# Kernel optimization log

Hardware: AMD Instinct MI355X
Metric: run time of the kernel (lower is better)

The kernel has to match this reference:

```python
import jax, jax.numpy as jnp
import numpy as np

B, T, D, H = 2, 4096, 768, 12
DH = D // H


def setup_inputs() -> dict:
    key = jax.random.key(0)
    ks = jax.random.split(key, 4)
    x = jax.random.normal(ks[0], (B, T, D), dtype=jnp.float32)
    Wqkv = jax.random.normal(ks[1], (D, 3 * D), dtype=jnp.float32) * (D ** -0.5)
    bqkv = jnp.zeros((3 * D,), dtype=jnp.float32)
    Wproj = jax.random.normal(ks[2], (D, D), dtype=jnp.float32) * (D ** -0.5)
    bproj = jnp.zeros((D,), dtype=jnp.float32)
    return {"x": x, "Wqkv": Wqkv, "bqkv": bqkv, "Wproj": Wproj, "bproj": bproj}


def reference(x, Wqkv, bqkv, Wproj, bproj):
    b, t, c = x.shape
    qkv = x @ Wqkv + bqkv                      # [B,T,3D]
    qkv = qkv.reshape(b, t, H, 3 * DH)
    q, k, v = jnp.split(qkv, 3, axis=-1)       # each [B,T,H,DH]
    q = q.transpose(0, 2, 1, 3)                # [B,H,T,DH]
    k = k.transpose(0, 2, 1, 3)
    v = v.transpose(0, 2, 1, 3)
    att = jnp.einsum('bhqd,bhkd->bhqk', q, k) / (DH ** 0.5)  # [B,H,T,T]
    mask = jnp.tril(jnp.ones((t, t), dtype=bool))
    att = jnp.where(mask, att, jnp.float32(-1e9))
    att = jax.nn.softmax(att, axis=-1)
    out = jnp.einsum('bhqk,bhkd->bhqd', att, v)  # [B,H,T,DH]
    out = out.transpose(0, 2, 1, 3).reshape(b, t, c)
    return out @ Wproj + bproj
```

## Files before the change

### kernel.cpp

```cpp
#include <hip/hip_runtime.h>

typedef unsigned short u16;
typedef unsigned int u32;
typedef __bf16 bf16x8 __attribute__((ext_vector_type(8)));
typedef float f32x4 __attribute__((ext_vector_type(4)));
typedef float f32x16 __attribute__((ext_vector_type(16)));
typedef u16 u16x4 __attribute__((ext_vector_type(4)));
typedef u32 u32x2 __attribute__((ext_vector_type(2)));
typedef u32 u32x4 __attribute__((ext_vector_type(4)));

#define QSCALE 0.18033688011112042f

static __device__ __forceinline__ u16 f2bf(float f) {
  __bf16 h = (__bf16)f;
  return __builtin_bit_cast(u16, h);
}

static __device__ __forceinline__ u32 pk2(float a, float b) {
  return (u32)f2bf(a) | ((u32)f2bf(b) << 16);
}

static __device__ __forceinline__ void gl_lds16(const void* g, void* l) {
  __builtin_amdgcn_global_load_lds(
      (const __attribute__((address_space(1))) unsigned int*)g,
      (__attribute__((address_space(3))) unsigned int*)l, 16, 0, 0);
}

static __device__ __forceinline__ f32x16 zero16() {
  f32x16 z;
#pragma unroll
  for (int i = 0; i < 16; ++i) z[i] = 0.f;
  return z;
}

__global__ void k_cvt(const float* __restrict__ in, u16* __restrict__ out, int n4) {
  int i = blockIdx.x * 256 + threadIdx.x;
  if (i < n4) {
    f32x4 f = ((const f32x4*)in)[i];
    u16x4 u = { f2bf(f[0]), f2bf(f[1]), f2bf(f[2]), f2bf(f[3]) };
    ((u16x4*)out)[i] = u;
  }
}

__global__ void k_transpose_cvt(const float* __restrict__ in, u16* __restrict__ out,
                                int R, int C) {
  __shared__ float tile[32][33];
  const int c0 = blockIdx.x * 32, r0 = blockIdx.y * 32;
  const int tx = threadIdx.x, ty = threadIdx.y;
#pragma unroll
  for (int i = 0; i < 4; ++i)
    tile[ty + i * 8][tx] = in[(size_t)(r0 + ty + i * 8) * C + c0 + tx];
  __syncthreads();
#pragma unroll
  for (int i = 0; i < 4; ++i)
    out[(size_t)(c0 + ty + i * 8) * R + r0 + tx] = f2bf(tile[tx][ty + i * 8]);
}

static __device__ __forceinline__ void gemm_core(const u16* __restrict__ Ag,
                                                 const u16* __restrict__ Btg,
                                                 int K, int m0, int n0,
                                                 u16* As, u16* Bs,
                                                 f32x4 acc[4][4]) {
  const int tid = threadIdx.x;
  const int lane = tid & 63;
  const int wid = tid >> 6;
  const int wm = wid >> 1, wn = wid & 1;
  const int l16 = lane & 15, lg = lane >> 4;

  for (int kt = 0; kt < K; kt += 64) {
    __syncthreads();
#pragma unroll
    for (int i = 0; i < 4; ++i) {
      int chunk = i * 256 + tid;
      int row = chunk >> 3;
      int lcb = ((chunk & 7) << 4) ^ ((row & 7) << 4);
      gl_lds16(Ag + (size_t)(m0 + row) * K + kt + (lcb >> 1),
               As + ((i * 256 + wid * 64) << 3));
    }
#pragma unroll
    for (int i = 0; i < 4; ++i) {
      int chunk = i * 256 + tid;
      int row = chunk >> 3;
      int lcb = ((chunk & 7) << 4) ^ ((row & 7) << 4);
      gl_lds16(Btg + (size_t)(n0 + row) * K + kt + (lcb >> 1),
               Bs + ((i * 256 + wid * 64) << 3));
    }
    __syncthreads();

#pragma unroll
    for (int ks = 0; ks < 2; ++ks) {
      bf16x8 af[4], bfr[4];
#pragma unroll
      for (int mi = 0; mi < 4; ++mi) {
        int row = wm * 64 + mi * 16 + l16;
        int off = row * 128 + ((ks * 64 + (lg << 4)) ^ ((row & 7) << 4));
        af[mi] = *(const bf16x8*)((const char*)As + off);
      }
#pragma unroll
      for (int ni = 0; ni < 4; ++ni) {
        int row = wn * 64 + ni * 16 + l16;
        int off = row * 128 + ((ks * 64 + (lg << 4)) ^ ((row & 7) << 4));
        bfr[ni] = *(const bf16x8*)((const char*)Bs + off);
      }
#pragma unroll
      for (int mi = 0; mi < 4; ++mi)
#pragma unroll
        for (int ni = 0; ni < 4; ++ni)
          acc[mi][ni] = __builtin_amdgcn_mfma_f32_16x16x32_bf16(
              af[mi], bfr[ni], acc[mi][ni], 0, 0, 0);
    }
  }
}

__global__ __launch_bounds__(256) void k_gemm_qkv(
    const u16* __restrict__ A, const u16* __restrict__ Bt,
    const float* __restrict__ bias, u16* __restrict__ Q, u16* __restrict__ Kb,
    u16* __restrict__ Vt) {
  __shared__ __align__(16) u16 As[128 * 64];
  __shared__ __align__(16) u16 Bs[128 * 64];
  const int m0 = blockIdx.y * 128, n0 = blockIdx.x * 128;
  const f32x4 fz = {0.f, 0.f, 0.f, 0.f};
  f32x4 acc[4][4];
#pragma unroll
  for (int mi = 0; mi < 4; ++mi)
#pragma unroll
    for (int ni = 0; ni < 4; ++ni) acc[mi][ni] = fz;

  gemm_core(A, Bt, 768, m0, n0, As, Bs, acc);

  const int tid = threadIdx.x, lane = tid & 63, wid = tid >> 6;
  const int wm = wid >> 1, wn = wid & 1, l16 = lane & 15, lg = lane >> 4;
#pragma unroll
  for (int mi = 0; mi < 4; ++mi)
#pragma unroll
    for (int ni = 0; ni < 4; ++ni) {
      int n = n0 + wn * 64 + ni * 16 + l16;
      float bi = bias[n];
      int h = n / 192;
      int rr = n - h * 192;
      int m0w = m0 + wm * 64 + mi * 16 + lg * 4;
      int bb = m0w >> 12, t0 = m0w & 4095;
      size_t base = ((size_t)(bb * 12 + h) * 4096 + t0) * 64;
      if (rr < 64) {
#pragma unroll
        for (int r = 0; r < 4; ++r)
          Q[base + (size_t)r * 64 + rr] = f2bf((acc[mi][ni][r] + bi) * QSCALE);
      } else if (rr < 128) {
#pragma unroll
        for (int r = 0; r < 4; ++r)
          Kb[base + (size_t)r * 64 + rr - 64] = f2bf(acc[mi][ni][r] + bi);
      } else {
        u16x4 vv;
#pragma unroll
        for (int r = 0; r < 4; ++r) vv[r] = f2bf(acc[mi][ni][r] + bi);
        *(u16x4*)(Vt + ((size_t)(bb * 12 + h) * 64 + (rr - 128)) * 4096 + t0) = vv;
      }
    }
}

__global__ __launch_bounds__(256) void k_gemm_proj(
    const u16* __restrict__ A, const u16* __restrict__ Bt,
    const float* __restrict__ bias, float* __restrict__ out) {
  __shared__ __align__(16) u16 As[128 * 64];
  __shared__ __align__(16) u16 Bs[128 * 64];
  const int m0 = blockIdx.y * 128, n0 = blockIdx.x * 128;
  const f32x4 fz = {0.f, 0.f, 0.f, 0.f};
  f32x4 acc[4][4];
#pragma unroll
  for (int mi = 0; mi < 4; ++mi)
#pragma unroll
    for (int ni = 0; ni < 4; ++ni) acc[mi][ni] = fz;

  gemm_core(A, Bt, 768, m0, n0, As, Bs, acc);

  const int tid = threadIdx.x, lane = tid & 63, wid = tid >> 6;
  const int wm = wid >> 1, wn = wid & 1, l16 = lane & 15, lg = lane >> 4;
#pragma unroll
  for (int mi = 0; mi < 4; ++mi)
#pragma unroll
    for (int ni = 0; ni < 4; ++ni) {
      int n = n0 + wn * 64 + ni * 16 + l16;
      float bi = bias[n];
#pragma unroll
      for (int r = 0; r < 4; ++r) {
        int m = m0 + wm * 64 + mi * 16 + lg * 4 + r;
        out[(size_t)m * 768 + n] = acc[mi][ni][r] + bi;
      }
    }
}

__global__ __launch_bounds__(128) void k_attn(const u16* __restrict__ Qg,
                                              const u16* __restrict__ Kg,
                                              const u16* __restrict__ Vtg,
                                              u16* __restrict__ Og) {
  __shared__ __align__(16) u16 Ks[2][64 * 64];
  __shared__ __align__(16) u16 Vs[2][64 * 64];
  const int bid = blockIdx.x;
  const int xcd = bid & 7;
  const int g = bid >> 3;
  const int bh = xcd * 3 + (g >> 6);
  const int jX = 63 - (g & 63);
  const int tid = threadIdx.x;
  const int lane = tid & 63;
  const int wid = tid >> 6;
  const int l32 = lane & 31;
  const int hi = lane >> 5;
  const int rxor = (l32 & 7) << 4;
  const size_t qk_base = (size_t)bh * (4096 * 64);
  const size_t vt_base = (size_t)bh * (64 * 4096);
  const int b = bh / 12, h = bh - b * 12;

  const int q0w = jX * 64 + wid * 32;
  const int qrow = q0w + l32;
  const int nkt = jX + 1;

  int coK[4], coVa[4], coVb[4];
#pragma unroll
  for (int st = 0; st < 4; ++st) coK[st] = (st * 32 + hi * 16) ^ rxor;
#pragma unroll
  for (int ks = 0; ks < 4; ++ks) {
    coVa[ks] = (ks * 32 + hi * 8) ^ rxor;
    coVb[ks] = (ks * 32 + 16 + hi * 8) ^ rxor;
  }
  const int rb0 = l32 * 128, rb1 = (32 + l32) * 128;

  const int trow = tid >> 3;
  const int tcol = ((((tid & 7) << 4) ^ ((trow & 7) << 4)) >> 1);
  const int tdst = tid << 3;
  const u16* kp0 = Kg + qk_base + (size_t)trow * 64 + tcol;
  const u16* kp1 = kp0 + (size_t)16 * 64;
  const u16* kp2 = kp0 + (size_t)32 * 64;
  const u16* kp3 = kp0 + (size_t)48 * 64;
  const u16* vq0 = Vtg + vt_base + (size_t)trow * 4096 + tcol;
  const u16* vq1 = vq0 + (size_t)16 * 4096;
  const u16* vq2 = vq0 + (size_t)32 * 4096;
  const u16* vq3 = vq0 + (size_t)48 * 4096;

  auto stage = [&](u16* Kd, u16* Vd) {
    gl_lds16(kp0, Kd + tdst);
    gl_lds16(kp1, Kd + 1024 + tdst);
    gl_lds16(kp2, Kd + 2048 + tdst);
    gl_lds16(kp3, Kd + 3072 + tdst);
    gl_lds16(vq0, Vd + tdst);
    gl_lds16(vq1, Vd + 1024 + tdst);
    gl_lds16(vq2, Vd + 2048 + tdst);
    gl_lds16(vq3, Vd + 3072 + tdst);
    kp0 += 4096; kp1 += 4096; kp2 += 4096; kp3 += 4096;
    vq0 += 64; vq1 += 64; vq2 += 64; vq3 += 64;
  };

  bf16x8 qb[4];
#pragma unroll
  for (int st = 0; st < 4; ++st)
    qb[st] = *(const bf16x8*)(Qg + qk_base + (size_t)qrow * 64 + st * 16 + hi * 8);

  f32x16 o0 = zero16(), o1 = zero16();
  float mrun = -3.0e38f, lrun = 0.f;

  stage(Ks[0], Vs[0]);
  __syncthreads();

  int cur = 0;
  for (int kt = 0; kt < nkt; ++kt) {
    if (kt + 1 < nkt) {
      stage(Ks[cur ^ 1], Vs[cur ^ 1]);
    }
    const bool diag = (kt == nkt - 1);
    const bool halfskip = diag && (wid == 0);
    const char* Kbp = (const char*)Ks[cur];
    const char* Vb = (const char*)Vs[cur];

    f32x16 s0 = zero16(), s1 = zero16();
    __builtin_amdgcn_s_setprio(1);
#pragma unroll
    for (int st = 0; st < 4; ++st) {
      bf16x8 ka0 = *(const bf16x8*)(Kbp + rb0 + coK[st]);
      s0 = __builtin_amdgcn_mfma_f32_32x32x16_bf16(ka0, qb[st], s0, 0, 0, 0);
    }
    if (!halfskip) {
#pragma unroll
      for (int st = 0; st < 4; ++st) {
        bf16x8 ka1 = *(const bf16x8*)(Kbp + rb1 + coK[st]);
        s1 = __builtin_amdgcn_mfma_f32_32x32x16_bf16(ka1, qb[st], s1, 0, 0, 0);
      }
    }
    __builtin_amdgcn_s_setprio(0);

    if (diag) {
      const int kbase = kt * 64 + 4 * hi;
#pragma unroll
      for (int r = 0; r < 16; ++r) {
        int kpv = kbase + (r & 3) + 8 * (r >> 2);
        s0[r] = (kpv > qrow) ? -3.0e38f : s0[r];
        if (!halfskip) s1[r] = (kpv + 32 > qrow) ? -3.0e38f : s1[r];
      }
    }

    float m8[8];
#pragma unroll
    for (int r = 0; r < 8; ++r) {
      float v = fmaxf(s0[r], s0[r + 8]);
      if (!halfskip) v = fmaxf(v, fmaxf(s1[r], s1[r + 8]));
      m8[r] = v;
    }
    float mx = fmaxf(fmaxf(fmaxf(m8[0], m8[1]), fmaxf(m8[2], m8[3])),
                     fmaxf(fmaxf(m8[4], m8[5]), fmaxf(m8[6], m8[7])));
    mx = fmaxf(mx, __shfl_xor(mx, 32, 64));

    if (__ballot(mx > mrun + 8.0f) != 0ull) {
      float mnew = fmaxf(mrun, mx);
      float al = __builtin_amdgcn_exp2f(mrun - mnew);
      o0 *= al;
      o1 *= al;
      lrun *= al;
      mrun = mnew;
    }

#pragma unroll
    for (int r = 0; r < 16; ++r) {
      s0[r] = __builtin_amdgcn_exp2f(s0[r] - mrun);
      if (!halfskip) s1[r] = __builtin_amdgcn_exp2f(s1[r] - mrun);
    }

    float a8[8];
#pragma unroll
    for (int r = 0; r < 8; ++r) {
      float v = s0[r] + s0[r + 8];
      if (!halfskip) v += s1[r] + s1[r + 8];
      a8[r] = v;
    }
    float rs = ((a8[0] + a8[1]) + (a8[2] + a8[3])) +
               ((a8[4] + a8[5]) + (a8[6] + a8[7]));
    rs += __shfl_xor(rs, 32, 64);
    lrun += rs;

    __builtin_amdgcn_s_setprio(1);
#pragma unroll
    for (int ks = 0; ks < 4; ++ks) {
      if (ks >= 2 && halfskip) continue;
      const f32x16& P = (ks >= 2) ? s1 : s0;
      const int base = (ks & 1) * 8;
      u32x4 w = { pk2(P[base + 0], P[base + 1]), pk2(P[base + 2], P[base + 3]),
                  pk2(P[base + 4], P[base + 5]), pk2(P[base + 6], P[base + 7]) };
      bf16x8 pbk = __builtin_bit_cast(bf16x8, w);
      u32x2 q0 = *(const u32x2*)(Vb + rb0 + coVa[ks]);
      u32x2 q1 = *(const u32x2*)(Vb + rb0 + coVb[ks]);
      u32x4 av = {q0[0], q0[1], q1[0], q1[1]};
      bf16x8 va0 = __builtin_bit_cast(bf16x8, av);
      o0 = __builtin_amdgcn_mfma_f32_32x32x16_bf16(va0, pbk, o0, 0, 0, 0);
      u32x2 p0 = *(const u32x2*)(Vb + rb1 + coVa[ks]);
      u32x2 p1 = *(const u32x2*)(Vb + rb1 + coVb[ks]);
      u32x4 bv = {p0[0], p0[1], p1[0], p1[1]};
      bf16x8 va1 = __builtin_bit_cast(bf16x8, bv);
      o1 = __builtin_amdgcn_mfma_f32_32x32x16_bf16(va1, pbk, o1, 0, 0, 0);
    }
    __builtin_amdgcn_s_setprio(0);

    __syncthreads();
    cur ^= 1;
  }

  float inv = 1.0f / lrun;
  u16* orow = Og + ((size_t)b * 4096 + qrow) * 768 + h * 64;
#pragma unroll
  for (int gg = 0; gg < 4; ++gg) {
    u16x4 v0, v1;
#pragma unroll
    for (int i = 0; i < 4; ++i) {
      v0[i] = f2bf(o0[4 * gg + i] * inv);
      v1[i] = f2bf(o1[4 * gg + i] * inv);
    }
    *(u16x4*)(orow + 8 * gg + 4 * hi) = v0;
    *(u16x4*)(orow + 32 + 8 * gg + 4 * hi) = v1;
  }
}

extern "C" void kernel_launch(void* const* d_in, const int* in_sizes, int n_in,
                              void* d_out, int out_size, void* d_ws, size_t ws_size,
                              hipStream_t stream) {
  const float* x = (const float*)d_in[0];
  const float* Wqkv = (const float*)d_in[1];
  const float* bqkv = (const float*)d_in[2];
  const float* Wproj = (const float*)d_in[3];
  const float* bproj = (const float*)d_in[4];
  float* out = (float*)d_out;

  char* ws = (char*)d_ws;
  u16* Xbf = (u16*)(ws + 0);
  u16* WqkvT = (u16*)(ws + 12582912);
  u16* WprojT = (u16*)(ws + 16121856);
  u16* Q = (u16*)(ws + 17301504);
  u16* K = (u16*)(ws + 29884416);
  u16* Vt = (u16*)(ws + 42467328);
  u16* O = (u16*)(ws + 55050240);

  k_cvt<<<6144, 256, 0, stream>>>(x, Xbf, 1572864);
  k_transpose_cvt<<<dim3(72, 24), dim3(32, 8), 0, stream>>>(Wqkv, WqkvT, 768, 2304);
  k_transpose_cvt<<<dim3(24, 24), dim3(32, 8), 0, stream>>>(Wproj, WprojT, 768, 768);
  k_gemm_qkv<<<dim3(18, 64), 256, 0, stream>>>(Xbf, WqkvT, bqkv, Q, K, Vt);
  k_attn<<<1536, 128, 0, stream>>>(Q, K, Vt, O);
  k_gemm_proj<<<dim3(6, 64), 256, 0, stream>>>(O, WprojT, bproj, out);
}
```

Measured before the change: 218.9 us.

## Split attention blocks into single-wave workgroups with vmcnt-based sync

The attention kernel now runs one 64-lane wave per workgroup, each owning 32 query rows, and launches twice as many workgroups. Because only one wave uses each LDS buffer, the __syncthreads barriers are replaced by explicit s_waitcnt vmcnt waits on the async global-to-LDS loads. The intent is to remove block-wide barrier stalls and give the scheduler finer-grained work for the causal imbalance. The cost is that each wave stages the full K/V tile on its own, doubling global-to-LDS traffic and LDS footprint per query row, which may lower occupancy.

```diff
diff --git a/kernel.cpp b/kernel.cpp
--- a/kernel.cpp
+++ b/kernel.cpp
@@ -24,6 +24,15 @@
   __builtin_amdgcn_global_load_lds(
       (const __attribute__((address_space(1))) unsigned int*)g,
       (__attribute__((address_space(3))) unsigned int*)l, 16, 0, 0);
+}
+
+static __device__ __forceinline__ void wait_vmcnt16() {
+  asm volatile("s_waitcnt vmcnt(16)" ::: "memory");
+  __builtin_amdgcn_sched_barrier(0);
+}
+static __device__ __forceinline__ void wait_vmcnt0() {
+  asm volatile("s_waitcnt vmcnt(0)" ::: "memory");
+  __builtin_amdgcn_sched_barrier(0);
 }
 
 static __device__ __forceinline__ f32x16 zero16() {
@@ -189,20 +198,18 @@
     }
 }
 
-__global__ __launch_bounds__(128) void k_attn(const u16* __restrict__ Qg,
-                                              const u16* __restrict__ Kg,
-                                              const u16* __restrict__ Vtg,
-                                              u16* __restrict__ Og) {
+__global__ __launch_bounds__(64) void k_attn(const u16* __restrict__ Qg,
+                                             const u16* __restrict__ Kg,
+                                             const u16* __restrict__ Vtg,
+                                             u16* __restrict__ Og) {
   __shared__ __align__(16) u16 Ks[2][64 * 64];
   __shared__ __align__(16) u16 Vs[2][64 * 64];
   const int bid = blockIdx.x;
   const int xcd = bid & 7;
   const int g = bid >> 3;
-  const int bh = xcd * 3 + (g >> 6);
-  const int jX = 63 - (g & 63);
-  const int tid = threadIdx.x;
-  const int lane = tid & 63;
-  const int wid = tid >> 6;
+  const int bh = xcd * 3 + (g >> 7);
+  const int jX = 127 - (g & 127);
+  const int lane = threadIdx.x;
   const int l32 = lane & 31;
   const int hi = lane >> 5;
   const int rxor = (l32 & 7) << 4;
@@ -210,9 +217,10 @@
   const size_t vt_base = (size_t)bh * (64 * 4096);
   const int b = bh / 12, h = bh - b * 12;
 
-  const int q0w = jX * 64 + wid * 32;
+  const int q0w = jX * 32;
   const int qrow = q0w + l32;
-  const int nkt = jX + 1;
+  const int nkt = (jX >> 1) + 1;
+  const bool hskip = ((jX & 1) == 0);
 
   int coK[4], coVa[4], coVb[4];
 #pragma unroll
@@ -224,29 +232,28 @@
   }
   const int rb0 = l32 * 128, rb1 = (32 + l32) * 128;
 
-  const int trow = tid >> 3;
-  const int tcol = ((((tid & 7) << 4) ^ ((trow & 7) << 4)) >> 1);
-  const int tdst = tid << 3;
-  const u16* kp0 = Kg + qk_base + (size_t)trow * 64 + tcol;
-  const u16* kp1 = kp0 + (size_t)16 * 64;
-  const u16* kp2 = kp0 + (size_t)32 * 64;
-  const u16* kp3 = kp0 + (size_t)48 * 64;
-  const u16* vq0 = Vtg + vt_base + (size_t)trow * 4096 + tcol;
-  const u16* vq1 = vq0 + (size_t)16 * 4096;
-  const u16* vq2 = vq0 + (size_t)32 * 4096;
-  const u16* vq3 = vq0 + (size_t)48 * 4096;
-
-  auto stage = [&](u16* Kd, u16* Vd) {
-    gl_lds16(kp0, Kd + tdst);
-    gl_lds16(kp1, Kd + 1024 + tdst);
-    gl_lds16(kp2, Kd + 2048 + tdst);
-    gl_lds16(kp3, Kd + 3072 + tdst);
-    gl_lds16(vq0, Vd + tdst);
-    gl_lds16(vq1, Vd + 1024 + tdst);
-    gl_lds16(vq2, Vd + 2048 + tdst);
-    gl_lds16(vq3, Vd + 3072 + tdst);
-    kp0 += 4096; kp1 += 4096; kp2 += 4096; kp3 += 4096;
-    vq0 += 64; vq1 += 64; vq2 += 64; vq3 += 64;
+  const int trow = lane >> 3;
+  const int tcol = ((((lane & 7) << 4) ^ (trow << 4)) >> 1);
+  const int tdst = lane << 3;
+  const u16* kp[8];
+  const u16* vq[8];
+#pragma unroll
+  for (int i = 0; i < 8; ++i) {
+    kp[i] = Kg + qk_base + (size_t)(i * 8 + trow) * 64 + tcol;
+    vq[i] = Vtg + vt_base + (size_t)(i * 8 + trow) * 4096 + tcol;
+  }
+
+  auto stage = [&](int buf) {
+#pragma unroll
+    for (int i = 0; i < 8; ++i) {
+      gl_lds16(kp[i], Ks[buf] + i * 512 + tdst);
+      kp[i] += 4096;
+    }
+#pragma unroll
+    for (int i = 0; i < 8; ++i) {
+      gl_lds16(vq[i], Vs[buf] + i * 512 + tdst);
+      vq[i] += 64;
+    }
   };
 
   bf16x8 qb[4];
@@ -257,16 +264,18 @@
   f32x16 o0 = zero16(), o1 = zero16();
   float mrun = -3.0e38f, lrun = 0.f;
 
-  stage(Ks[0], Vs[0]);
-  __syncthreads();
+  stage(0);
 
   int cur = 0;
   for (int kt = 0; kt < nkt; ++kt) {
     if (kt + 1 < nkt) {
-      stage(Ks[cur ^ 1], Vs[cur ^ 1]);
+      stage(cur ^ 1);
+      wait_vmcnt16();
+    } else {
+      wait_vmcnt0();
     }
     const bool diag = (kt == nkt - 1);
-    const bool halfskip = diag && (wid == 0);
+    const bool halfskip = diag && hskip;
     const char* Kbp = (const char*)Ks[cur];
     const char* Vb = (const char*)Vs[cur];
 
@@ -356,7 +365,6 @@
     }
     __builtin_amdgcn_s_setprio(0);
 
-    __syncthreads();
     cur ^= 1;
   }
 
@@ -398,6 +406,6 @@
   k_transpose_cvt<<<dim3(72, 24), dim3(32, 8), 0, stream>>>(Wqkv, WqkvT, 768, 2304);
   k_transpose_cvt<<<dim3(24, 24), dim3(32, 8), 0, stream>>>(Wproj, WprojT, 768, 768);
   k_gemm_qkv<<<dim3(18, 64), 256, 0, stream>>>(Xbf, WqkvT, bqkv, Q, K, Vt);
-  k_attn<<<1536, 128, 0, stream>>>(Q, K, Vt, O);
+  k_attn<<<3072, 64, 0, stream>>>(Q, K, Vt, O);
   k_gemm_proj<<<dim3(6, 64), 256, 0, stream>>>(O, WprojT, bproj, out);
 }
```

After: 284.0 us. 1.3x slower.
